# Performance work log

Hardware: AMD Instinct MI355X
Metric: run time of the kernel (lower is better)

## Reference

```python
import jax, jax.numpy as jnp
import numpy as np

B, N, D = 8, 900, 256
SA_H, CA_H = 8, 8
L, P = 4, 4
FF = 2048
SHAPES = ((128, 128), (64, 64), (32, 32), (16, 16))
STARTS = (0, 16384, 20480, 21504)
S = 21760
D_BAND = (D // 6) * 2   # 84
D_ROPE = 3 * D_BAND     # 252
NF = D_BAND // 2        # 42
EPS = 1e-5


def _ln(x, g, b):
    mu = jnp.mean(x, -1, keepdims=True)
    var = jnp.mean((x - mu) ** 2, -1, keepdims=True)
    return (x - mu) * jax.lax.rsqrt(var + EPS) * g + b


def _rotate_half(x):
    x1 = x[..., 0::2]
    x2 = x[..., 1::2]
    return jnp.stack([-x2, x1], axis=-1).reshape(x.shape)


def _rope(q, k, boxes):
    freqs = 1.0 / (10000.0 ** (jnp.arange(NF, dtype=jnp.float32) / NF))
    cx, cy = boxes[..., 0], boxes[..., 1]
    xy = cx * cy

    def cs(v, f):
        a = v[..., None] * f
        return jnp.repeat(jnp.cos(a), 2, -1), jnp.repeat(jnp.sin(a), 2, -1)

    cx_c, cx_s = cs(cx, freqs)
    cy_c, cy_s = cs(cy, freqs)
    xy_c, xy_s = cs(xy, freqs * 0.1)
    cos = jnp.concatenate([cx_c, cy_c, xy_c], -1)
    sin = jnp.concatenate([cx_s, cy_s, xy_s], -1)

    def app(t):
        a, rest = t[..., :D_ROPE], t[..., D_ROPE:]
        return jnp.concatenate([a * cos + _rotate_half(a) * sin, rest], -1)

    return app(q), app(k)


def _bilinear(img, xy):
    # img: (Hl, Wl, C); xy: (M, 2) normalized in [0,1]
    # torch grid_sample semantics: align_corners=False, zero padding
    Hl, Wl, _ = img.shape
    x = xy[:, 0] * Wl - 0.5
    y = xy[:, 1] * Hl - 0.5
    x0 = jnp.floor(x)
    y0 = jnp.floor(y)
    lx = x - x0
    ly = y - y0
    x0i = x0.astype(jnp.int32)
    y0i = y0.astype(jnp.int32)

    def tap(yi, xi):
        valid = (xi >= 0) & (xi < Wl) & (yi >= 0) & (yi < Hl)
        v = img[jnp.clip(yi, 0, Hl - 1), jnp.clip(xi, 0, Wl - 1)]
        return v * valid[:, None].astype(v.dtype)

    return (tap(y0i, x0i) * ((1 - ly) * (1 - lx))[:, None]
            + tap(y0i, x0i + 1) * ((1 - ly) * lx)[:, None]
            + tap(y0i + 1, x0i) * (ly * (1 - lx))[:, None]
            + tap(y0i + 1, x0i + 1) * (ly * lx)[:, None])


def _forward(tgt, memory, query_pos, ref_boxes, reference_points,
             wq, bq, wk, bk, wv, bv, sa_wo, sa_bo, n1_g, n1_b,
             off_w, off_b, aw_w, aw_b, val_w, val_b, co_w, co_b,
             n2_g, n2_b, ff1_w, ff1_b, ff2_w, ff2_b, n3_g, n3_b):
    dh = D // SA_H
    # --- self attention with ComplexRoPE2D applied pre-projection ---
    q = tgt + query_pos
    k = tgt + query_pos
    q, k = _rope(q, k, ref_boxes)
    qh = (q @ wq + bq).reshape(B, N, SA_H, dh).transpose(0, 2, 1, 3)
    kh = (k @ wk + bk).reshape(B, N, SA_H, dh).transpose(0, 2, 1, 3)
    vh = (tgt @ wv + bv).reshape(B, N, SA_H, dh).transpose(0, 2, 1, 3)
    att = jax.nn.softmax(jnp.einsum('bhqd,bhkd->bhqk', qh, kh) * (dh ** -0.5), axis=-1)
    sa = jnp.einsum('bhqk,bhkd->bhqd', att, vh).transpose(0, 2, 1, 3).reshape(B, N, D)
    tgt = _ln(tgt + sa @ sa_wo + sa_bo, n1_g, n1_b)

    # --- multi-scale deformable cross-attention ---
    cdh = D // CA_H
    q2 = tgt + query_pos
    value = (memory @ val_w + val_b).reshape(B, S, CA_H, cdh)
    off = (q2 @ off_w + off_b).reshape(B, N, CA_H, L, P, 2)
    aw = jax.nn.softmax((q2 @ aw_w + aw_b).reshape(B, N, CA_H, L * P), axis=-1)
    aw = aw.reshape(B, N, CA_H, L, P)
    # offset normalizer is (W, H) per level
    normalizer = jnp.array([[w_, h_] for (h_, w_) in SHAPES], dtype=jnp.float32)
    loc = reference_points[:, :, None, :, None, :] + off / normalizer[None, None, None, :, None, :]
    out = jnp.zeros((B, CA_H, N, cdh), dtype=tgt.dtype)
    for l, (Hl, Wl) in enumerate(SHAPES):
        st = STARTS[l]
        v_l = value[:, st:st + Hl * Wl].reshape(B, Hl, Wl, CA_H, cdh)
        v_l = v_l.transpose(0, 3, 1, 2, 4).reshape(B * CA_H, Hl, Wl, cdh)
        loc_l = loc[:, :, :, l].transpose(0, 2, 1, 3, 4).reshape(B * CA_H, N * P, 2)
        s_l = jax.vmap(_bilinear)(v_l, loc_l).reshape(B, CA_H, N, P, cdh)
        out = out + jnp.einsum('bhnpd,bnhp->bhnd', s_l, aw[:, :, :, l])
    ca = out.transpose(0, 2, 1, 3).reshape(B, N, D) @ co_w + co_b
    tgt = _ln(tgt + ca, n2_g, n2_b)

    # --- FFN ---
    ff = jax.nn.relu(tgt @ ff1_w + ff1_b) @ ff2_w + ff2_b
    return _ln(tgt + ff, n3_g, n3_b)


def setup_inputs() -> dict:
    key = jax.random.key(0)
    ks = jax.random.split(key, 16)

    def wmat(k, shape):
        return jax.random.normal(k, shape, jnp.float32) * 0.02

    z = lambda *s: jnp.zeros(s, jnp.float32)
    o = lambda *s: jnp.ones(s, jnp.float32)
    return dict(
        tgt=jax.random.normal(ks[0], (B, N, D), jnp.float32),
        memory=jax.random.normal(ks[1], (B, S, D), jnp.float32),
        query_pos=jax.random.normal(ks[2], (B, N, D), jnp.float32) * 0.02,
        ref_boxes=jax.random.uniform(ks[3], (B, N, 4), jnp.float32),
        reference_points=jax.random.uniform(ks[4], (B, N, L, 2), jnp.float32),
        wq=wmat(ks[5], (D, D)), bq=z(D),
        wk=wmat(ks[6], (D, D)), bk=z(D),
        wv=wmat(ks[7], (D, D)), bv=z(D),
        sa_wo=wmat(ks[8], (D, D)), sa_bo=z(D),
        n1_g=o(D), n1_b=z(D),
        off_w=wmat(ks[9], (D, CA_H * L * P * 2)), off_b=z(CA_H * L * P * 2),
        aw_w=wmat(ks[10], (D, CA_H * L * P)), aw_b=z(CA_H * L * P),
        val_w=wmat(ks[11], (D, D)), val_b=z(D),
        co_w=wmat(ks[12], (D, D)), co_b=z(D),
        n2_g=o(D), n2_b=z(D),
        ff1_w=wmat(ks[13], (D, FF)), ff1_b=z(FF),
        ff2_w=wmat(ks[14], (FF, D)), ff2_b=z(D),
        n3_g=o(D), n3_b=z(D))


def reference(tgt, memory, query_pos, ref_boxes, reference_points,
              wq, bq, wk, bk, wv, bv, sa_wo, sa_bo, n1_g, n1_b,
              off_w, off_b, aw_w, aw_b, val_w, val_b, co_w, co_b,
              n2_g, n2_b, ff1_w, ff1_b, ff2_w, ff2_b, n3_g, n3_b):
    return _forward(tgt, memory, query_pos, ref_boxes, reference_points,
                    wq, bq, wk, bk, wv, bv, sa_wo, sa_bo, n1_g, n1_b,
                    off_w, off_b, aw_w, aw_b, val_w, val_b, co_w, co_b,
                    n2_g, n2_b, ff1_w, ff1_b, ff2_w, ff2_b, n3_g, n3_b)
```

## Files before the change

### kernel.cpp

```cpp
#include <hip/hip_runtime.h>
#include <hip/hip_bf16.h>
#include <math.h>

#define B_ 8
#define N_ 900
#define D_ 256
#define S_ 21760
#define H_ 8
#define DH 32
#define FF_ 2048
#define NROWS (B_*N_)

typedef __attribute__((ext_vector_type(8))) short bf16x8;
typedef __attribute__((ext_vector_type(4))) float f32x4;

union BU { bf16x8 v; short s[8]; unsigned long long u[2]; };

static __device__ inline short f2bf_s(float x) {
  __hip_bfloat16 h = __float2bfloat16(x);
  return *reinterpret_cast<short*>(&h);
}

__device__ __forceinline__ void gload_lds16(const float* g, float* lds) {
  __builtin_amdgcn_global_load_lds(
      (const __attribute__((address_space(1))) void*)g,
      (__attribute__((address_space(3))) void*)lds, 16, 0, 0);
}

__global__ __launch_bounds__(128) void rope_kernel(
    const float* __restrict__ tgt, const float* __restrict__ qpos,
    const float* __restrict__ boxes, float* __restrict__ out)
{
  int row = blockIdx.x;
  int tid = threadIdx.x;
  const float* x = tgt  + (size_t)row * D_;
  const float* p = qpos + (size_t)row * D_;
  float a0 = x[2*tid]   + p[2*tid];
  float a1 = x[2*tid+1] + p[2*tid+1];
  float o0 = a0, o1 = a1;
  if (tid < 126) {
    int band = tid / 42;
    int fi   = tid - band * 42;
    float freq = powf(10000.0f, -(float)fi / 42.0f);
    float cx = boxes[(size_t)row*4 + 0];
    float cy = boxes[(size_t)row*4 + 1];
    float v  = (band == 0) ? cx : (band == 1 ? cy : cx * cy);
    if (band == 2) freq *= 0.1f;
    float ang = v * freq;
    float c = cosf(ang), s = sinf(ang);
    o0 = a0 * c - a1 * s;
    o1 = a1 * c + a0 * s;
  }
  out[(size_t)row*D_ + 2*tid]   = o0;
  out[(size_t)row*D_ + 2*tid+1] = o1;
}

__global__ __launch_bounds__(256) void wtrans_kernel(
    const float* __restrict__ wq, const float* __restrict__ wk,
    const float* __restrict__ wv, const float* __restrict__ sa_wo,
    const float* __restrict__ offw, const float* __restrict__ valw,
    const float* __restrict__ cow, const float* __restrict__ aww,
    const float* __restrict__ ff1w, const float* __restrict__ ff2w,
    short* __restrict__ Wt)
{
  int bid = blockIdx.x;
  const float* W; short* out; int K, N, tile;
  if (bid < 448) {
    int wi = bid >> 6; tile = bid & 63; K = 256; N = 256;
    const float* tab[7] = {wq, wk, wv, sa_wo, offw, valw, cow};
    const int   off[7]  = {0, 65536, 131072, 196608, 262144, 360448, 425984};
    W = tab[wi]; out = Wt + off[wi];
  } else if (bid < 480) {
    tile = bid - 448; K = 256; N = 128; W = aww; out = Wt + 327680;
  } else if (bid < 992) {
    tile = bid - 480; K = 256; N = 2048; W = ff1w; out = Wt + 491520;
  } else {
    tile = bid - 992; K = 2048; N = 256; W = ff2w; out = Wt + 1015808;
  }
  int ntn = N >> 5;
  int tk = tile / ntn, tn = tile - tk * ntn;
  __shared__ float t[32][33];
  int c = threadIdx.x & 31, rr = threadIdx.x >> 5;
  #pragma unroll
  for (int i = 0; i < 4; ++i)
    t[rr + i*8][c] = W[(size_t)(tk*32 + rr + i*8) * N + tn*32 + c];
  __syncthreads();
  #pragma unroll
  for (int i = 0; i < 4; ++i)
    out[(size_t)(tn*32 + rr + i*8) * K + tk*32 + c] = f2bf_s(t[c][rr + i*8]);
}

template<int BM, int KK, bool ABF16, bool A2ADD, bool RELU, int OUTMODE>
__global__ __launch_bounds__(256) void mgemm_kernel(
    const void* __restrict__ Ap, const float* __restrict__ A2p,
    const short* __restrict__ Wt,
    const float* __restrict__ bias, const float* __restrict__ bias2,
    void* __restrict__ Cp, void* __restrict__ Cp2, int M, int N)
{
  constexpr int MS = BM / 16;
  constexpr bool SWAP = (OUTMODE != 2);
  __shared__ short As[BM * 256];
  int tid = threadIdx.x;
  int w = tid >> 6, lane = tid & 63;
  int g = lane >> 4, r = lane & 15;
  int m0 = blockIdx.x * BM;
  int nw = blockIdx.y * 256 + w * 64;
  bool active = nw < N;

  f32x4 acc[MS][4];
  #pragma unroll
  for (int i = 0; i < MS; ++i)
    #pragma unroll
    for (int j = 0; j < 4; ++j) acc[i][j] = (f32x4){0.f,0.f,0.f,0.f};

  for (int kb = 0; kb < KK; kb += 256) {
    if (KK > 256 && kb) __syncthreads();
    #pragma unroll
    for (int i = 0; i < BM/8; ++i) {
      int u = i*256 + tid;
      int row = u >> 5, c8 = u & 31;
      BU pk;
      if (ABF16) {
        pk.v = *(const bf16x8*)((const short*)Ap + (size_t)(m0+row)*KK + kb + c8*8);
      } else {
        const float* ap = (const float*)Ap + (size_t)(m0+row)*KK + kb + c8*8;
        float4 a0 = *(const float4*)ap;
        float4 a1 = *(const float4*)(ap + 4);
        if (A2ADD) {
          const float* a2 = A2p + (size_t)(m0+row)*KK + kb + c8*8;
          float4 b0 = *(const float4*)a2;
          float4 b1 = *(const float4*)(a2 + 4);
          a0.x += b0.x; a0.y += b0.y; a0.z += b0.z; a0.w += b0.w;
          a1.x += b1.x; a1.y += b1.y; a1.z += b1.z; a1.w += b1.w;
        }
        pk.s[0]=f2bf_s(a0.x); pk.s[1]=f2bf_s(a0.y); pk.s[2]=f2bf_s(a0.z); pk.s[3]=f2bf_s(a0.w);
        pk.s[4]=f2bf_s(a1.x); pk.s[5]=f2bf_s(a1.y); pk.s[6]=f2bf_s(a1.z); pk.s[7]=f2bf_s(a1.w);
      }
      int col = (c8*8) ^ ((row & 7) << 3);
      *(bf16x8*)&As[row*256 + col] = pk.v;
    }
    __syncthreads();
    if (active) {
      #pragma unroll
      for (int kk = 0; kk < 8; ++kk) {
        BU bfr[4];
        #pragma unroll
        for (int ns = 0; ns < 4; ++ns) {
          const short* wp = Wt + (size_t)(nw + ns*16 + r)*KK + kb + kk*32;
          bfr[ns].u[0] = *(const unsigned long long*)(wp + 4*g);
          bfr[ns].u[1] = *(const unsigned long long*)(wp + 16 + 4*g);
        }
        #pragma unroll
        for (int ms = 0; ms < MS; ++ms) {
          int row = ms*16 + r;
          int c0 = (kk*32 + g*4)      ^ ((r & 7) << 3);
          int c1 = (kk*32 + 16 + g*4) ^ ((r & 7) << 3);
          BU af;
          af.u[0] = *(const unsigned long long*)&As[row*256 + c0];
          af.u[1] = *(const unsigned long long*)&As[row*256 + c1];
          #pragma unroll
          for (int ns = 0; ns < 4; ++ns) {
            if (SWAP)
              acc[ms][ns] = __builtin_amdgcn_mfma_f32_16x16x32_bf16(
                  bfr[ns].v, af.v, acc[ms][ns], 0, 0, 0);
            else
              acc[ms][ns] = __builtin_amdgcn_mfma_f32_16x16x32_bf16(
                  af.v, bfr[ns].v, acc[ms][ns], 0, 0, 0);
          }
        }
      }
    }
  }
  if (!active) return;

  #pragma unroll
  for (int ms = 0; ms < MS; ++ms) {
    #pragma unroll
    for (int ns = 0; ns < 4; ++ns) {
      if (SWAP) {
        int n0 = nw + ns*16 + g*4;
        int m  = m0 + ms*16 + r;
        float4 b4;
        if (OUTMODE == 3 || OUTMODE == 4)
          b4 = (n0 < 256) ? *(const float4*)&bias[n0]
                          : *(const float4*)&bias2[n0 - 256];
        else
          b4 = *(const float4*)&bias[n0];
        float v0 = acc[ms][ns][0] + b4.x;
        float v1 = acc[ms][ns][1] + b4.y;
        float v2 = acc[ms][ns][2] + b4.z;
        float v3 = acc[ms][ns][3] + b4.w;
        if (RELU) {
          v0 = fmaxf(v0, 0.f); v1 = fmaxf(v1, 0.f);
          v2 = fmaxf(v2, 0.f); v3 = fmaxf(v3, 0.f);
        }
        if (OUTMODE == 0) {
          *(float4*)&((float*)Cp)[(size_t)m*N + n0] = make_float4(v0,v1,v2,v3);
        } else if (OUTMODE == 1) {
          short4 sv = make_short4(f2bf_s(v0), f2bf_s(v1), f2bf_s(v2), f2bf_s(v3));
          *(short4*)&((short*)Cp)[(size_t)m*N + n0] = sv;
        } else if (OUTMODE == 3) {
          short4 sv = make_short4(f2bf_s(v0), f2bf_s(v1), f2bf_s(v2), f2bf_s(v3));
          if (n0 < 256) *(short4*)&((short*)Cp )[(size_t)m*256 + n0]       = sv;
          else          *(short4*)&((short*)Cp2)[(size_t)m*256 + (n0-256)] = sv;
        } else {
          float4 fv = make_float4(v0,v1,v2,v3);
          if (n0 < 256) *(float4*)&((float*)Cp )[(size_t)m*256 + n0]       = fv;
          else          *(float4*)&((float*)Cp2)[(size_t)m*128 + (n0-256)] = fv;
        }
      } else {
        int n = nw + ns*16 + r;
        float bsc = bias[n];
        int hh = n >> 5, dd = n & 31;
        int mb = m0 + ms*16 + g*4;
        short4 sv = make_short4(
            f2bf_s(acc[ms][ns][0] + bsc), f2bf_s(acc[ms][ns][1] + bsc),
            f2bf_s(acc[ms][ns][2] + bsc), f2bf_s(acc[ms][ns][3] + bsc));
        int bb = mb / N_, bbe = (mb + 3) / N_;
        if (bb == bbe) {
          int nn = mb - bb * N_;
          *(short4*)&((short*)Cp)[((size_t)((bb*H_ + hh)*DH + dd))*N_ + nn] = sv;
        } else {
          const short* sp = (const short*)&sv;
          #pragma unroll
          for (int j = 0; j < 4; ++j) {
            int m = mb + j;
            int b2 = m / N_, nn = m - b2 * N_;
            ((short*)Cp)[((size_t)((b2*H_ + hh)*DH + dd))*N_ + nn] = sp[j];
          }
        }
      }
    }
  }
}

__global__ __launch_bounds__(256) void vgemm_kernel(
    const float* __restrict__ Ap, const short* __restrict__ Wt,
    const float* __restrict__ bias, short* __restrict__ Cp)
{
  __shared__ float buf[8][1024];
  __shared__ float dump[1024];
  int tid = threadIdx.x;
  int w = tid >> 6, l = tid & 63;
  int g = l >> 4, r = l & 15;
  int nw = w * 64;

  BU wreg[4][8];
  #pragma unroll
  for (int ns = 0; ns < 4; ++ns) {
    const short* wp = Wt + (size_t)(nw + ns*16 + r) * 256;
    #pragma unroll
    for (int kk = 0; kk < 8; ++kk) {
      wreg[ns][kk].u[0] = *(const unsigned long long*)(wp + kk*32 + 4*g);
      wreg[ns][kk].u[1] = *(const unsigned long long*)(wp + kk*32 + 16 + 4*g);
    }
  }
  float4 bs4[4];
  #pragma unroll
  for (int ns = 0; ns < 4; ++ns) bs4[ns] = *(const float4*)&bias[nw + ns*16 + g*4];

  int srow = w*8 + (l >> 3);
  int schunk = (l & 7) ^ (srow & 7);
  const float* gbase = Ap + ((size_t)blockIdx.x*160 + srow) * 256 + schunk*4;

  #pragma unroll
  for (int t = 0; t < 6; ++t)
    gload_lds16(gbase + (t>>3)*8192 + (t&7)*32, &buf[t][w*256]);

  f32x4 acc[2][4];
  #pragma unroll
  for (int i = 0; i < 2; ++i)
    #pragma unroll
    for (int j = 0; j < 4; ++j) acc[i][j] = (f32x4){0.f,0.f,0.f,0.f};

  for (int s = 0; s < 5; ++s) {
    #pragma unroll
    for (int c = 0; c < 8; ++c) {
      int t = s*8 + c;
      int tn = t + 6;
      if (tn < 40) gload_lds16(gbase + (tn>>3)*8192 + (tn&7)*32,
                               &buf[(c+6)&7][w*256]);
      else         gload_lds16(gbase, &dump[w*256]);
      asm volatile("s_waitcnt vmcnt(6)" ::: "memory");
      __builtin_amdgcn_s_barrier();
      const float* bp = &buf[c][0];
      #pragma unroll
      for (int ms = 0; ms < 2; ++ms) {
        int row = ms*16 + r;
        const float* rp = bp + row*32;
        float4 f0 = *(const float4*)&rp[((g    ) ^ (row & 7)) * 4];
        float4 f1 = *(const float4*)&rp[((g + 4) ^ (row & 7)) * 4];
        BU af;
        af.s[0]=f2bf_s(f0.x); af.s[1]=f2bf_s(f0.y); af.s[2]=f2bf_s(f0.z); af.s[3]=f2bf_s(f0.w);
        af.s[4]=f2bf_s(f1.x); af.s[5]=f2bf_s(f1.y); af.s[6]=f2bf_s(f1.z); af.s[7]=f2bf_s(f1.w);
        #pragma unroll
        for (int ns = 0; ns < 4; ++ns)
          acc[ms][ns] = __builtin_amdgcn_mfma_f32_16x16x32_bf16(
              wreg[ns][c].v, af.v, acc[ms][ns], 0, 0, 0);
      }
    }
    int m0 = blockIdx.x*160 + s*32;
    #pragma unroll
    for (int ms = 0; ms < 2; ++ms) {
      #pragma unroll
      for (int ns = 0; ns < 4; ++ns) {
        int m  = m0 + ms*16 + r;
        int n0 = nw + ns*16 + g*4;
        short4 sv = make_short4(
            f2bf_s(acc[ms][ns][0] + bs4[ns].x),
            f2bf_s(acc[ms][ns][1] + bs4[ns].y),
            f2bf_s(acc[ms][ns][2] + bs4[ns].z),
            f2bf_s(acc[ms][ns][3] + bs4[ns].w));
        *(short4*)&Cp[(size_t)m*256 + n0] = sv;
        acc[ms][ns] = (f32x4){0.f,0.f,0.f,0.f};
      }
    }
  }
}

__global__ __launch_bounds__(64) void mfma_attn_kernel(
    const __hip_bfloat16* __restrict__ Q,
    const __hip_bfloat16* __restrict__ K,
    const __hip_bfloat16* __restrict__ Vt,
    float* __restrict__ O)
{
  const int NQT = 57;
  int wid = blockIdx.x;
  int qt = wid % NQT, bh = wid / NQT;
  int b = bh >> 3, h = bh & 7;
  int lane = threadIdx.x;
  int g = lane >> 4, r = lane & 15;
  int q0 = qt * 16;
  const float scale = 0.17677669529663687f;

  union U { bf16x8 v; short s[8]; unsigned long long u64[2]; };

  U qf;
  {
    int qrow = min(q0 + r, N_ - 1);
    const __hip_bfloat16* qp = Q + ((size_t)(b*N_ + qrow))*D_ + h*DH;
    qf.u64[0] = *(const unsigned long long*)(qp + 4*g);
    qf.u64[1] = *(const unsigned long long*)(qp + 16 + 4*g);
  }

  f32x4 oacc0 = {0.f,0.f,0.f,0.f};
  f32x4 oacc1 = {0.f,0.f,0.f,0.f};
  float m = -1e30f, l = 0.0f;
  const f32x4 zero = {0.f,0.f,0.f,0.f};

  const __hip_bfloat16* vbase0 = Vt + (size_t)(bh*DH + r) * N_;
  const __hip_bfloat16* vbase1 = Vt + (size_t)(bh*DH + 16 + r) * N_;

  for (int kt = 0; kt < N_; kt += 32) {
    U kf0, kf1;
    {
      int kr0 = min(kt + r, N_ - 1);
      int kr1 = min(kt + 16 + r, N_ - 1);
      const __hip_bfloat16* kp0 = K + ((size_t)(b*N_ + kr0))*D_ + h*DH;
      const __hip_bfloat16* kp1 = K + ((size_t)(b*N_ + kr1))*D_ + h*DH;
      kf0.u64[0] = *(const unsigned long long*)(kp0 + 4*g);
      kf0.u64[1] = *(const unsigned long long*)(kp0 + 16 + 4*g);
      kf1.u64[0] = *(const unsigned long long*)(kp1 + 4*g);
      kf1.u64[1] = *(const unsigned long long*)(kp1 + 16 + 4*g);
    }
    f32x4 s0 = __builtin_amdgcn_mfma_f32_16x16x32_bf16(kf0.v, qf.v, zero, 0, 0, 0);
    f32x4 s1 = __builtin_amdgcn_mfma_f32_16x16x32_bf16(kf1.v, qf.v, zero, 0, 0, 0);

    float sc[8];
    #pragma unroll
    for (int j = 0; j < 4; ++j) {
      sc[j]   = (kt + 4*g + j      < N_) ? s0[j] * scale : -1e30f;
      sc[4+j] = (kt + 16 + 4*g + j < N_) ? s1[j] * scale : -1e30f;
    }
    float mx = sc[0];
    #pragma unroll
    for (int j = 1; j < 8; ++j) mx = fmaxf(mx, sc[j]);
    mx = fmaxf(mx, __shfl_xor(mx, 16));
    mx = fmaxf(mx, __shfl_xor(mx, 32));

    float mnew = fmaxf(m, mx);
    float corr = __expf(m - mnew);
    float p[8], ps = 0.f;
    #pragma unroll
    for (int j = 0; j < 8; ++j) { p[j] = __expf(sc[j] - mnew); ps += p[j]; }
    ps += __shfl_xor(ps, 16);
    ps += __shfl_xor(ps, 32);
    l = l * corr + ps;
    m = mnew;
    #pragma unroll
    for (int j = 0; j < 4; ++j) { oacc0[j] *= corr; oacc1[j] *= corr; }

    U pf;
    #pragma unroll
    for (int j = 0; j < 8; ++j) pf.s[j] = f2bf_s(p[j]);

    U vf0, vf1;
    vf0.u64[0] = *(const unsigned long long*)(vbase0 + kt + 4*g);
    vf0.u64[1] = *(const unsigned long long*)(vbase0 + kt + 16 + 4*g);
    vf1.u64[0] = *(const unsigned long long*)(vbase1 + kt + 4*g);
    vf1.u64[1] = *(const unsigned long long*)(vbase1 + kt + 16 + 4*g);

    oacc0 = __builtin_amdgcn_mfma_f32_16x16x32_bf16(vf0.v, pf.v, oacc0, 0, 0, 0);
    oacc1 = __builtin_amdgcn_mfma_f32_16x16x32_bf16(vf1.v, pf.v, oacc1, 0, 0, 0);
  }

  if (q0 + r < N_) {
    float inv = 1.0f / l;
    float* op = O + ((size_t)(b*N_ + q0 + r))*D_ + h*DH;
    #pragma unroll
    for (int j = 0; j < 4; ++j) {
      op[4*g + j]      = oacc0[j] * inv;
      op[16 + 4*g + j] = oacc1[j] * inv;
    }
  }
}

__global__ __launch_bounds__(256) void add_ln_kernel(
    const float* __restrict__ X, const float* __restrict__ Y,
    const float* __restrict__ g, const float* __restrict__ beta,
    float* __restrict__ out)
{
  int row = blockIdx.x, tid = threadIdx.x;
  float v = X[(size_t)row*D_ + tid] + Y[(size_t)row*D_ + tid];
  float s = v, s2 = v*v;
  #pragma unroll
  for (int off = 32; off; off >>= 1) {
    s  += __shfl_down(s,  off, 64);
    s2 += __shfl_down(s2, off, 64);
  }
  __shared__ float red[8];
  int wid = tid >> 6, lane = tid & 63;
  if (lane == 0) { red[wid] = s; red[wid+4] = s2; }
  __syncthreads();
  if (tid == 0) {
    float ts  = red[0]+red[1]+red[2]+red[3];
    float ts2 = red[4]+red[5]+red[6]+red[7];
    float mu  = ts * (1.0f/D_);
    float var = ts2 * (1.0f/D_) - mu*mu;
    red[0] = mu;
    red[1] = rsqrtf(fmaxf(var, 0.0f) + 1e-5f);
  }
  __syncthreads();
  float mu = red[0], rr = red[1];
  out[(size_t)row*D_ + tid] = (v - mu)*rr*g[tid] + beta[tid];
}

__global__ __launch_bounds__(256) void sample4_kernel(
    const __hip_bfloat16* __restrict__ V, const float* __restrict__ offp,
    const float* __restrict__ awl, const float* __restrict__ refp,
    float* __restrict__ out)
{
  int tid = threadIdx.x;
  int q = tid >> 6, t = tid & 63;
  int row = blockIdx.x * 4 + q;
  int b = row / N_;
  __shared__ float s_aw[4][128];
  __shared__ float s_loc[4][256];
  #pragma unroll
  for (int i = 0; i < 2; ++i)
    s_aw[q][t + i*64] = awl[(size_t)row*128 + t + i*64];
  {
    const float norms[4] = {128.f, 64.f, 32.f, 16.f};
    #pragma unroll
    for (int i = 0; i < 4; ++i) {
      int e = t + i*64;
      int rem = e & 31, li = rem >> 3, ax = rem & 1;
      s_loc[q][e] = refp[((size_t)row*4 + li)*2 + ax]
                  + offp[(size_t)row*256 + e] / norms[li];
    }
  }
  __syncthreads();
  if (t < 8) {
    float mx = -1e30f;
    for (int j = 0; j < 16; ++j) mx = fmaxf(mx, s_aw[q][t*16+j]);
    float sum = 0.f;
    for (int j = 0; j < 16; ++j) sum += __expf(s_aw[q][t*16+j] - mx);
    float inv = 1.0f / sum;
    for (int j = 0; j < 16; ++j)
      s_aw[q][t*16+j] = __expf(s_aw[q][t*16+j] - mx) * inv;
  }
  __syncthreads();
  int h = t >> 3, dq = t & 7;
  const int dims[4]   = {128, 64, 32, 16};
  const int starts[4] = {0, 16384, 20480, 21504};
  const __hip_bfloat16* Vb = V + ((size_t)b*S_)*D_ + h*DH + dq*4;
  float a0 = 0.f, a1 = 0.f, a2 = 0.f, a3 = 0.f;
  #pragma unroll
  for (int l = 0; l < 4; ++l) {
    int Wl = dims[l], st = starts[l];
    #pragma unroll
    for (int p = 0; p < 4; ++p) {
      float lx = s_loc[q][h*32 + l*8 + p*2 + 0];
      float ly = s_loc[q][h*32 + l*8 + p*2 + 1];
      float x = lx * Wl - 0.5f, y = ly * Wl - 0.5f;
      float x0f = floorf(x), y0f = floorf(y);
      float fx = x - x0f, fy = y - y0f;
      int x0 = (int)x0f, y0 = (int)y0f;
      float v0 = 0.f, v1 = 0.f, v2 = 0.f, v3 = 0.f;
      #pragma unroll
      for (int ty = 0; ty < 2; ++ty) {
        int yi = y0 + ty;
        float wy = ty ? fy : (1.f - fy);
        if (yi < 0 || yi >= Wl) continue;
        #pragma unroll
        for (int txi = 0; txi < 2; ++txi) {
          int xi = x0 + txi;
          float wx = txi ? fx : (1.f - fx);
          if (xi < 0 || xi >= Wl) continue;
          unsigned long long vv =
              *(const unsigned long long*)&Vb[(size_t)(st + yi*Wl + xi) * D_];
          float ww = wy * wx;
          v0 += ww * __uint_as_float((unsigned)(vv) << 16);
          v1 += ww * __uint_as_float((unsigned)(vv) & 0xffff0000u);
          v2 += ww * __uint_as_float((unsigned)(vv >> 32) << 16);
          v3 += ww * __uint_as_float((unsigned)(vv >> 32) & 0xffff0000u);
        }
      }
      float aw = s_aw[q][h*16 + l*4 + p];
      a0 += aw * v0; a1 += aw * v1; a2 += aw * v2; a3 += aw * v3;
    }
  }
  float4 res = make_float4(a0, a1, a2, a3);
  *(float4*)&out[(size_t)row*D_ + h*DH + dq*4] = res;
}

extern "C" void kernel_launch(void* const* d_in, const int* in_sizes, int n_in,
                              void* d_out, int out_size, void* d_ws, size_t ws_size,
                              hipStream_t stream)
{
  const float* tgt    = (const float*)d_in[0];
  const float* memory = (const float*)d_in[1];
  const float* qpos   = (const float*)d_in[2];
  const float* boxes  = (const float*)d_in[3];
  const float* refp   = (const float*)d_in[4];
  const float* wq = (const float*)d_in[5];   const float* bq = (const float*)d_in[6];
  const float* wk = (const float*)d_in[7];   const float* bk = (const float*)d_in[8];
  const float* wv = (const float*)d_in[9];   const float* bv = (const float*)d_in[10];
  const float* sa_wo = (const float*)d_in[11]; const float* sa_bo = (const float*)d_in[12];
  const float* n1g = (const float*)d_in[13]; const float* n1b = (const float*)d_in[14];
  const float* off_w = (const float*)d_in[15]; const float* off_b = (const float*)d_in[16];
  const float* aw_w  = (const float*)d_in[17]; const float* aw_b  = (const float*)d_in[18];
  const float* val_w = (const float*)d_in[19]; const float* val_b = (const float*)d_in[20];
  const float* co_w  = (const float*)d_in[21]; const float* co_b  = (const float*)d_in[22];
  const float* n2g = (const float*)d_in[23]; const float* n2b = (const float*)d_in[24];
  const float* ff1_w = (const float*)d_in[25]; const float* ff1_b = (const float*)d_in[26];
  const float* ff2_w = (const float*)d_in[27]; const float* ff2_b = (const float*)d_in[28];
  const float* n3g = (const float*)d_in[29]; const float* n3b = (const float*)d_in[30];

  char* ws = (char*)d_ws;
  size_t NE = (size_t)NROWS * D_;
  __hip_bfloat16* Vv = (__hip_bfloat16*)ws;
  __hip_bfloat16* FFM = (__hip_bfloat16*)ws;
  size_t p = (size_t)B_ * S_ * D_ * sizeof(__hip_bfloat16);
  float* A  = (float*)(ws + p); p += NE*4;
  float* Qb = (float*)(ws + p); p += NE*4;
  float* Kb = (float*)(ws + p); p += NE*4;
  float* Vh = (float*)(ws + p); p += NE*4;
  float* S1 = (float*)(ws + p); p += NE*4;
  float* S2 = (float*)(ws + p); p += NE*4;
  float* T1 = (float*)(ws + p); p += NE*4;
  short* Wt = (short*)((char*)Kb + NE*2);
  float* out = (float*)d_out;
  (void)ws_size; (void)in_sizes; (void)n_in; (void)out_size;

  const short* qk_t  = Wt;
  const short* wv_t  = Wt + 131072;
  const short* sa_t  = Wt + 196608;
  const short* offaw_t = Wt + 262144;
  const short* val_t = Wt + 360448;
  const short* co_t  = Wt + 425984;
  const short* ff1_t = Wt + 491520;
  const short* ff2_t = Wt + 1015808;

  wtrans_kernel<<<1504, 256, 0, stream>>>(wq, wk, wv, sa_wo, off_w, val_w,
                                          co_w, aw_w, ff1_w, ff2_w, Wt);

  rope_kernel<<<NROWS, 128, 0, stream>>>(tgt, qpos, boxes, A);
  mgemm_kernel<32,256,false,false,false,3><<<dim3(225,2), 256, 0, stream>>>(
      A, nullptr, qk_t, bq, bk, Qb, Kb, NROWS, 512);
  mgemm_kernel<32,256,false,false,false,2><<<dim3(225,1), 256, 0, stream>>>(
      tgt, nullptr, wv_t, bv, nullptr, Vh, nullptr, NROWS, 256);
  mfma_attn_kernel<<<57 * B_ * H_, 64, 0, stream>>>(
      (const __hip_bfloat16*)Qb, (const __hip_bfloat16*)Kb,
      (const __hip_bfloat16*)Vh, S1);
  mgemm_kernel<32,256,false,false,false,0><<<dim3(225,1), 256, 0, stream>>>(
      S1, nullptr, sa_t, sa_bo, nullptr, S2, nullptr, NROWS, 256);
  add_ln_kernel<<<NROWS, 256, 0, stream>>>(tgt, S2, n1g, n1b, T1);

  vgemm_kernel<<<1088, 256, 0, stream>>>(memory, val_t, val_b, (short*)Vv);
  mgemm_kernel<32,256,false,true,false,4><<<dim3(225,2), 256, 0, stream>>>(
      T1, qpos, offaw_t, off_b, aw_b, Qb, Kb, NROWS, 384);
  sample4_kernel<<<NROWS/4, 256, 0, stream>>>(Vv, Qb, Kb, refp, S1);
  mgemm_kernel<32,256,false,false,false,0><<<dim3(225,1), 256, 0, stream>>>(
      S1, nullptr, co_t, co_b, nullptr, S2, nullptr, NROWS, 256);
  add_ln_kernel<<<NROWS, 256, 0, stream>>>(T1, S2, n2g, n2b, T1);

  mgemm_kernel<32,256,false,false,true,1><<<dim3(225,8), 256, 0, stream>>>(
      T1, nullptr, ff1_t, ff1_b, nullptr, FFM, nullptr, NROWS, FF_);
  mgemm_kernel<32,2048,true,false,false,0><<<dim3(225,1), 256, 0, stream>>>(
      FFM, nullptr, ff2_t, ff2_b, nullptr, S2, nullptr, NROWS, 256);
  add_ln_kernel<<<NROWS, 256, 0, stream>>>(T1, S2, n3g, n3b, out);
}
```

Measured before the change: 472.9 us.

## Store value projection head-major, emit bf16 rope output, tile attention over 32 queries

The value-projection GEMM now writes memory values in a per-batch, per-head [pixel][32] layout, so each bilinear tap in the sampling kernel reads from a compact head-contiguous region instead of a 256-wide row. The rope kernel writes bf16 instead of fp32, and the QK GEMM is switched to its bf16-input variant, which halves that intermediate's traffic. The attention kernel handles 32 queries per wave instead of 16, so each K/V fragment load is reused for two query tiles and the grid shrinks. The risks are higher register pressure in attention and fewer waves in flight.

```diff
diff --git a/kernel.cpp b/kernel.cpp
--- a/kernel.cpp
+++ b/kernel.cpp
@@ -29,7 +29,7 @@
 
 __global__ __launch_bounds__(128) void rope_kernel(
     const float* __restrict__ tgt, const float* __restrict__ qpos,
-    const float* __restrict__ boxes, float* __restrict__ out)
+    const float* __restrict__ boxes, __hip_bfloat16* __restrict__ out)
 {
   int row = blockIdx.x;
   int tid = threadIdx.x;
@@ -51,8 +51,8 @@
     o0 = a0 * c - a1 * s;
     o1 = a1 * c + a0 * s;
   }
-  out[(size_t)row*D_ + 2*tid]   = o0;
-  out[(size_t)row*D_ + 2*tid+1] = o1;
+  short2 sv = make_short2(f2bf_s(o0), f2bf_s(o1));
+  *(short2*)&out[(size_t)row*D_ + 2*tid] = sv;
 }
 
 __global__ __launch_bounds__(256) void wtrans_kernel(
@@ -273,6 +273,9 @@
     #pragma unroll
     for (int j = 0; j < 4; ++j) acc[i][j] = (f32x4){0.f,0.f,0.f,0.f};
 
+  int bb = blockIdx.x / 136;
+  int pixblk = (blockIdx.x % 136) * 160;
+
   for (int s = 0; s < 5; ++s) {
     #pragma unroll
     for (int c = 0; c < 8; ++c) {
@@ -299,19 +302,20 @@
               wreg[ns][c].v, af.v, acc[ms][ns], 0, 0, 0);
       }
     }
-    int m0 = blockIdx.x*160 + s*32;
+    int pix0 = pixblk + s*32;
     #pragma unroll
     for (int ms = 0; ms < 2; ++ms) {
       #pragma unroll
       for (int ns = 0; ns < 4; ++ns) {
-        int m  = m0 + ms*16 + r;
-        int n0 = nw + ns*16 + g*4;
+        int pix = pix0 + ms*16 + r;
+        int n0  = nw + ns*16 + g*4;
+        int hh = n0 >> 5, dd = n0 & 31;
         short4 sv = make_short4(
             f2bf_s(acc[ms][ns][0] + bs4[ns].x),
             f2bf_s(acc[ms][ns][1] + bs4[ns].y),
             f2bf_s(acc[ms][ns][2] + bs4[ns].z),
             f2bf_s(acc[ms][ns][3] + bs4[ns].w));
-        *(short4*)&Cp[(size_t)m*256 + n0] = sv;
+        *(short4*)&Cp[((size_t)(bb*H_ + hh)*S_ + pix)*32 + dd] = sv;
         acc[ms][ns] = (f32x4){0.f,0.f,0.f,0.f};
       }
     }
@@ -324,28 +328,33 @@
     const __hip_bfloat16* __restrict__ Vt,
     float* __restrict__ O)
 {
-  const int NQT = 57;
+  const int NQT = 29;
   int wid = blockIdx.x;
   int qt = wid % NQT, bh = wid / NQT;
   int b = bh >> 3, h = bh & 7;
   int lane = threadIdx.x;
   int g = lane >> 4, r = lane & 15;
-  int q0 = qt * 16;
+  int q0 = qt * 32;
   const float scale = 0.17677669529663687f;
 
   union U { bf16x8 v; short s[8]; unsigned long long u64[2]; };
 
-  U qf;
-  {
-    int qrow = min(q0 + r, N_ - 1);
+  U qf[2];
+  #pragma unroll
+  for (int qq = 0; qq < 2; ++qq) {
+    int qrow = min(q0 + qq*16 + r, N_ - 1);
     const __hip_bfloat16* qp = Q + ((size_t)(b*N_ + qrow))*D_ + h*DH;
-    qf.u64[0] = *(const unsigned long long*)(qp + 4*g);
-    qf.u64[1] = *(const unsigned long long*)(qp + 16 + 4*g);
-  }
-
-  f32x4 oacc0 = {0.f,0.f,0.f,0.f};
-  f32x4 oacc1 = {0.f,0.f,0.f,0.f};
-  float m = -1e30f, l = 0.0f;
+    qf[qq].u64[0] = *(const unsigned long long*)(qp + 4*g);
+    qf[qq].u64[1] = *(const unsigned long long*)(qp + 16 + 4*g);
+  }
+
+  f32x4 oaccA[2], oaccB[2];
+  #pragma unroll
+  for (int qq = 0; qq < 2; ++qq) {
+    oaccA[qq] = (f32x4){0.f,0.f,0.f,0.f};
+    oaccB[qq] = (f32x4){0.f,0.f,0.f,0.f};
+  }
+  float m0v = -1e30f, m1v = -1e30f, l0v = 0.f, l1v = 0.f;
   const f32x4 zero = {0.f,0.f,0.f,0.f};
 
   const __hip_bfloat16* vbase0 = Vt + (size_t)(bh*DH + r) * N_;
@@ -363,54 +372,63 @@
       kf1.u64[0] = *(const unsigned long long*)(kp1 + 4*g);
       kf1.u64[1] = *(const unsigned long long*)(kp1 + 16 + 4*g);
     }
-    f32x4 s0 = __builtin_amdgcn_mfma_f32_16x16x32_bf16(kf0.v, qf.v, zero, 0, 0, 0);
-    f32x4 s1 = __builtin_amdgcn_mfma_f32_16x16x32_bf16(kf1.v, qf.v, zero, 0, 0, 0);
-
-    float sc[8];
-    #pragma unroll
-    for (int j = 0; j < 4; ++j) {
-      sc[j]   = (kt + 4*g + j      < N_) ? s0[j] * scale : -1e30f;
-      sc[4+j] = (kt + 16 + 4*g + j < N_) ? s1[j] * scale : -1e30f;
-    }
-    float mx = sc[0];
-    #pragma unroll
-    for (int j = 1; j < 8; ++j) mx = fmaxf(mx, sc[j]);
-    mx = fmaxf(mx, __shfl_xor(mx, 16));
-    mx = fmaxf(mx, __shfl_xor(mx, 32));
-
-    float mnew = fmaxf(m, mx);
-    float corr = __expf(m - mnew);
-    float p[8], ps = 0.f;
-    #pragma unroll
-    for (int j = 0; j < 8; ++j) { p[j] = __expf(sc[j] - mnew); ps += p[j]; }
-    ps += __shfl_xor(ps, 16);
-    ps += __shfl_xor(ps, 32);
-    l = l * corr + ps;
-    m = mnew;
-    #pragma unroll
-    for (int j = 0; j < 4; ++j) { oacc0[j] *= corr; oacc1[j] *= corr; }
-
-    U pf;
-    #pragma unroll
-    for (int j = 0; j < 8; ++j) pf.s[j] = f2bf_s(p[j]);
-
     U vf0, vf1;
     vf0.u64[0] = *(const unsigned long long*)(vbase0 + kt + 4*g);
     vf0.u64[1] = *(const unsigned long long*)(vbase0 + kt + 16 + 4*g);
     vf1.u64[0] = *(const unsigned long long*)(vbase1 + kt + 4*g);
     vf1.u64[1] = *(const unsigned long long*)(vbase1 + kt + 16 + 4*g);
 
-    oacc0 = __builtin_amdgcn_mfma_f32_16x16x32_bf16(vf0.v, pf.v, oacc0, 0, 0, 0);
-    oacc1 = __builtin_amdgcn_mfma_f32_16x16x32_bf16(vf1.v, pf.v, oacc1, 0, 0, 0);
-  }
-
-  if (q0 + r < N_) {
-    float inv = 1.0f / l;
-    float* op = O + ((size_t)(b*N_ + q0 + r))*D_ + h*DH;
-    #pragma unroll
-    for (int j = 0; j < 4; ++j) {
-      op[4*g + j]      = oacc0[j] * inv;
-      op[16 + 4*g + j] = oacc1[j] * inv;
+    #pragma unroll
+    for (int qq = 0; qq < 2; ++qq) {
+      f32x4 s0 = __builtin_amdgcn_mfma_f32_16x16x32_bf16(kf0.v, qf[qq].v, zero, 0, 0, 0);
+      f32x4 s1 = __builtin_amdgcn_mfma_f32_16x16x32_bf16(kf1.v, qf[qq].v, zero, 0, 0, 0);
+      float m = qq ? m1v : m0v;
+      float lv = qq ? l1v : l0v;
+
+      float sc[8];
+      #pragma unroll
+      for (int j = 0; j < 4; ++j) {
+        sc[j]   = (kt + 4*g + j      < N_) ? s0[j] * scale : -1e30f;
+        sc[4+j] = (kt + 16 + 4*g + j < N_) ? s1[j] * scale : -1e30f;
+      }
+      float mx = sc[0];
+      #pragma unroll
+      for (int j = 1; j < 8; ++j) mx = fmaxf(mx, sc[j]);
+      mx = fmaxf(mx, __shfl_xor(mx, 16));
+      mx = fmaxf(mx, __shfl_xor(mx, 32));
+
+      float mnew = fmaxf(m, mx);
+      float corr = __expf(m - mnew);
+      float p[8], ps = 0.f;
+      #pragma unroll
+      for (int j = 0; j < 8; ++j) { p[j] = __expf(sc[j] - mnew); ps += p[j]; }
+      ps += __shfl_xor(ps, 16);
+      ps += __shfl_xor(ps, 32);
+      lv = lv * corr + ps;
+      if (qq) { m1v = mnew; l1v = lv; } else { m0v = mnew; l0v = lv; }
+      #pragma unroll
+      for (int j = 0; j < 4; ++j) { oaccA[qq][j] *= corr; oaccB[qq][j] *= corr; }
+
+      U pf;
+      #pragma unroll
+      for (int j = 0; j < 8; ++j) pf.s[j] = f2bf_s(p[j]);
+
+      oaccA[qq] = __builtin_amdgcn_mfma_f32_16x16x32_bf16(vf0.v, pf.v, oaccA[qq], 0, 0, 0);
+      oaccB[qq] = __builtin_amdgcn_mfma_f32_16x16x32_bf16(vf1.v, pf.v, oaccB[qq], 0, 0, 0);
+    }
+  }
+
+  #pragma unroll
+  for (int qq = 0; qq < 2; ++qq) {
+    int qrow = q0 + qq*16 + r;
+    if (qrow < N_) {
+      float inv = 1.0f / (qq ? l1v : l0v);
+      float* op = O + ((size_t)(b*N_ + qrow))*D_ + h*DH;
+      #pragma unroll
+      for (int j = 0; j < 4; ++j) {
+        op[4*g + j]      = oaccA[qq][j] * inv;
+        op[16 + 4*g + j] = oaccB[qq][j] * inv;
+      }
     }
   }
 }
@@ -483,7 +501,7 @@
   int h = t >> 3, dq = t & 7;
   const int dims[4]   = {128, 64, 32, 16};
   const int starts[4] = {0, 16384, 20480, 21504};
-  const __hip_bfloat16* Vb = V + ((size_t)b*S_)*D_ + h*DH + dq*4;
+  const __hip_bfloat16* Vb = V + ((size_t)(b*H_ + h) * S_) * 32 + dq*4;
   float a0 = 0.f, a1 = 0.f, a2 = 0.f, a3 = 0.f;
   #pragma unroll
   for (int l = 0; l < 4; ++l) {
@@ -508,7 +526,7 @@
           float wx = txi ? fx : (1.f - fx);
           if (xi < 0 || xi >= Wl) continue;
           unsigned long long vv =
-              *(const unsigned long long*)&Vb[(size_t)(st + yi*Wl + xi) * D_];
+              *(const unsigned long long*)&Vb[(size_t)(st + yi*Wl + xi) * 32];
           float ww = wy * wx;
           v0 += ww * __uint_as_float((unsigned)(vv) << 16);
           v1 += ww * __uint_as_float((unsigned)(vv) & 0xffff0000u);
@@ -575,12 +593,12 @@
   wtrans_kernel<<<1504, 256, 0, stream>>>(wq, wk, wv, sa_wo, off_w, val_w,
                                           co_w, aw_w, ff1_w, ff2_w, Wt);
 
-  rope_kernel<<<NROWS, 128, 0, stream>>>(tgt, qpos, boxes, A);
-  mgemm_kernel<32,256,false,false,false,3><<<dim3(225,2), 256, 0, stream>>>(
+  rope_kernel<<<NROWS, 128, 0, stream>>>(tgt, qpos, boxes, (__hip_bfloat16*)A);
+  mgemm_kernel<32,256,true,false,false,3><<<dim3(225,2), 256, 0, stream>>>(
       A, nullptr, qk_t, bq, bk, Qb, Kb, NROWS, 512);
   mgemm_kernel<32,256,false,false,false,2><<<dim3(225,1), 256, 0, stream>>>(
       tgt, nullptr, wv_t, bv, nullptr, Vh, nullptr, NROWS, 256);
-  mfma_attn_kernel<<<57 * B_ * H_, 64, 0, stream>>>(
+  mfma_attn_kernel<<<29 * B_ * H_, 64, 0, stream>>>(
       (const __hip_bfloat16*)Qb, (const __hip_bfloat16*)Kb,
       (const __hip_bfloat16*)Vh, S1);
   mgemm_kernel<32,256,false,false,false,0><<<dim3(225,1), 256, 0, stream>>>(
```

Result: faster. 438.4 us (-7.3%).
